# Kernel tuning notes

Hardware: AMD Instinct MI355X
Metric: run time of the kernel (lower is better)

## Reference

```python
import jax, jax.numpy as jnp
import numpy as np


def setup_inputs() -> dict:
    key = jax.random.key(0)
    k_q, k_k, k_v, k_xd, k_yd = jax.random.split(key, 5)
    B, L, H, E, K = 8, 4096, 2048, 512, 64
    return {
        "queries": jax.random.normal(k_q, (B, L, E), dtype=jnp.float32),
        "keys": jax.random.normal(k_k, (B, L, E), dtype=jnp.float32),
        "values": jax.random.normal(k_v, (B, L, E), dtype=jnp.float32),
        "x_date": jax.random.normal(k_xd, (B, L, K), dtype=jnp.float32),
        "y_date": jax.random.normal(k_yd, (B, H, K), dtype=jnp.float32),
    }


def reference(queries, keys, values, x_date, y_date):
    # queries/keys are unused in the original forward's math (only shapes).
    k = x_date.shape[-1]
    scale = 1.0 / float(np.sqrt(k))  # self.scale is None -> 1/sqrt(k)
    # scores: [B, L, H] from date features
    scores = jnp.einsum('blk,bhk->blh', x_date, y_date)
    # softmax over target axis H (dim=-1), numerically stable
    A = jax.nn.softmax(scale * scores, axis=-1)  # [B, L, H]
    # weighted reduction over source axis L -> [B, H, E]
    V = jnp.einsum('ble,blh->bhe', values, A)
    return V
```

## Files before the change

kernel.cpp:

```cpp
#include <hip/hip_runtime.h>
#include <hip/hip_bf16.h>

#define BN 8
#define LN 4096
#define HN 2048
#define EN 512
#define KN 64
#define LT 32

typedef __attribute__((ext_vector_type(8))) short bf16x8;
typedef __attribute__((ext_vector_type(4))) float f32x4;

__device__ __forceinline__ short f2b(float x) {
  union { float f; unsigned u; } v; v.f = x;
  unsigned r = v.u + 0x7fffu + ((v.u >> 16) & 1u);
  return (short)(r >> 16);
}

__device__ __forceinline__ void gload16(const void* g, void* s) {
  __builtin_amdgcn_global_load_lds(
      (const __attribute__((address_space(1))) unsigned int*)(unsigned long long)g,
      (__attribute__((address_space(3))) unsigned int*)(unsigned int)(unsigned long long)s,
      16, 0, 0);
}

__global__ __launch_bounds__(256) void prep_cvt(const float* __restrict__ src,
                                                short* __restrict__ dst, float scale) {
  int i = blockIdx.x * 256 + threadIdx.x;
  f32x4 a = *(const f32x4*)(src + (size_t)i * 8);
  f32x4 b = *(const f32x4*)(src + (size_t)i * 8 + 4);
  bf16x8 r;
  r[0] = f2b(a[0] * scale); r[1] = f2b(a[1] * scale);
  r[2] = f2b(a[2] * scale); r[3] = f2b(a[3] * scale);
  r[4] = f2b(b[0] * scale); r[5] = f2b(b[1] * scale);
  r[6] = f2b(b[2] * scale); r[7] = f2b(b[3] * scale);
  *(bf16x8*)(dst + (size_t)i * 8) = r;
}

__global__ __launch_bounds__(256) void prep_v(const float* __restrict__ vals,
                                              short* __restrict__ valsT) {
  __shared__ short tile[64 * 66];
  const int b = blockIdx.z;
  const int l0 = blockIdx.x * 64, e0 = blockIdx.y * 64;
  const int tid = threadIdx.x;
  {
    int lr = tid >> 2, ec = (tid & 3) * 16;
    const float* src = vals + ((size_t)b * LN + l0 + lr) * EN + e0 + ec;
    short* trow = tile + lr * 66 + ec;
#pragma unroll
    for (int q = 0; q < 4; ++q) {
      f32x4 v = *(const f32x4*)(src + q * 4);
      unsigned u0 = (unsigned)(unsigned short)f2b(v[0]) | ((unsigned)(unsigned short)f2b(v[1]) << 16);
      unsigned u1 = (unsigned)(unsigned short)f2b(v[2]) | ((unsigned)(unsigned short)f2b(v[3]) << 16);
      *(unsigned*)(trow + q * 4) = u0;
      *(unsigned*)(trow + q * 4 + 2) = u1;
    }
  }
  __syncthreads();
  {
    int er = tid >> 2, lc = (tid & 3) * 16;
    union { short s[16]; bf16x8 v[2]; } u;
#pragma unroll
    for (int k2 = 0; k2 < 16; ++k2) u.s[k2] = tile[(lc + k2) * 66 + er];
    short* dst = valsT + ((size_t)b * EN + e0 + er) * LN + l0 + lc;
    *(bf16x8*)dst = u.v[0];
    *(bf16x8*)(dst + 8) = u.v[1];
  }
}

__global__ __launch_bounds__(256) void k_stats2(const short* __restrict__ xb,
                                                const short* __restrict__ yb,
                                                float* __restrict__ ps) {
  const int b = blockIdx.y, hc = blockIdx.z;
  const int tid = threadIdx.x, w = tid >> 6, lane = tid & 63;
  const int row = lane & 15, g = lane >> 4;
  const int lb = blockIdx.x * 128 + w * 32;
  const size_t bL = (size_t)b * LN, bH = (size_t)b * HN;

  bf16x8 xa[2][2];
#pragma unroll
  for (int lt = 0; lt < 2; ++lt) {
    const short* xp = xb + ((bL + lb + lt * 16 + row) << 6) + 8 * g;
    xa[lt][0] = *(const bf16x8*)xp;
    xa[lt][1] = *(const bf16x8*)(xp + 32);
  }
  float s[2][4] = {{0.f, 0.f, 0.f, 0.f}, {0.f, 0.f, 0.f, 0.f}};
  const short* ybase = yb + ((bH + hc * 512 + row) << 6) + 8 * g;
#pragma unroll 2
  for (int it = 0; it < 32; ++it) {
    const short* yp = ybase + ((size_t)it << 10);
    bf16x8 y0 = *(const bf16x8*)yp;
    bf16x8 y1 = *(const bf16x8*)(yp + 32);
#pragma unroll
    for (int lt = 0; lt < 2; ++lt) {
      f32x4 a = {0.f, 0.f, 0.f, 0.f};
      a = __builtin_amdgcn_mfma_f32_16x16x32_bf16(xa[lt][0], y0, a, 0, 0, 0);
      a = __builtin_amdgcn_mfma_f32_16x16x32_bf16(xa[lt][1], y1, a, 0, 0, 0);
#pragma unroll
      for (int r = 0; r < 4; ++r) s[lt][r] += __builtin_amdgcn_exp2f(a[r]);
    }
  }
#pragma unroll
  for (int d = 1; d < 16; d <<= 1)
#pragma unroll
    for (int lt = 0; lt < 2; ++lt)
#pragma unroll
      for (int r = 0; r < 4; ++r) s[lt][r] += __shfl_xor(s[lt][r], d);
  if (row == 0) {
#pragma unroll
    for (int lt = 0; lt < 2; ++lt)
#pragma unroll
      for (int r = 0; r < 4; ++r)
        ps[(size_t)hc * (BN * LN) + bL + lb + lt * 16 + 4 * g + r] = s[lt][r];
  }
}

__global__ void k_comb(const float* __restrict__ ps, float* __restrict__ wv) {
  int idx = blockIdx.x * 256 + threadIdx.x;
  float z = ps[idx] + ps[BN * LN + idx] + ps[2 * BN * LN + idx] + ps[3 * BN * LN + idx];
  wv[idx] = 1.0f / z;
}

__global__ __launch_bounds__(256, 4) void k_main2(
    const short* __restrict__ valsT, const short* __restrict__ xb,
    const short* __restrict__ yb, const float* __restrict__ wv,
    float* __restrict__ out) {
  __shared__ __align__(16) char smem[33024];
  const int tid = threadIdx.x;
  const int lane = tid & 63, w = tid >> 6;
  const int row = lane & 15, g = lane >> 4;

  int flat = blockIdx.x + 32 * blockIdx.y + 128 * blockIdx.z;
  int re = (flat & 7) * 128 + (flat >> 3);
  const int hb = (re & 31) * 64;
  const int eb = ((re >> 5) & 3) * 128;
  const int b = re >> 7;
  const size_t bL = (size_t)b * LN, bH = (size_t)b * HN;

  bf16x8 ya[2][2];
#pragma unroll
  for (int j2 = 0; j2 < 2; ++j2) {
    const short* yp = yb + ((bH + hb + ((w >> 1) * 2 + j2) * 16 + row) << 6) + 8 * g;
    ya[j2][0] = *(const bf16x8*)yp;
    ya[j2][1] = *(const bf16x8*)(yp + 32);
  }

  f32x4 acc[2][4];
#pragma unroll
  for (int at = 0; at < 2; ++at)
#pragma unroll
    for (int n = 0; n < 4; ++n) acc[at][n] = (f32x4){0.f, 0.f, 0.f, 0.f};

  const int wbase = __builtin_amdgcn_readfirstlane(tid & ~63);

  auto stage = [&](int buf, int l0n) {
#pragma unroll
    for (int j = 0; j < 2; ++j) {
      int i = j * 256 + tid;
      int e = i >> 2, sl = (i & 3) ^ ((e >> 1) & 3);
      const short* src = valsT + (((size_t)b * EN + eb + e) << 12) + l0n + 8 * sl;
      gload16(src, smem + buf * 8192 + (j * 256 + wbase) * 16);
    }
    {
      int l = tid >> 3, sl = (tid & 7) ^ (l & 7);
      const short* src = xb + ((bL + l0n + l) << 6) + 8 * sl;
      gload16(src, smem + 16384 + buf * 4096 + wbase * 16);
    }
    if (tid < 8) {
      gload16(wv + bL + l0n + 4 * tid, smem + 32768 + buf * 128);
    }
  };

  stage(0, 0);
  __syncthreads();

  const int t = w & 1, hp = w >> 1;
  int cur = 0;
  for (int it = 0; it < LN / LT; ++it) {
    int l0 = it * LT;
    if (it + 1 < LN / LT) stage(cur ^ 1, l0 + LT);

    short* xT = (short*)(smem + 16384 + cur * 4096);
    char* pT = smem + 24576 + cur * 4096;
    float* sw = (float*)(smem + 32768 + cur * 128);

    int sp0 = g ^ (row & 7);
    const short* xrow = xT + ((t * 16 + row) << 6);
    bf16x8 xa0 = *(const bf16x8*)(xrow + (sp0 << 3));
    bf16x8 xa1 = *(const bf16x8*)(xrow + ((sp0 ^ 4) << 3));
    float swv[4];
#pragma unroll
    for (int r = 0; r < 4; ++r) swv[r] = sw[t * 16 + 4 * g + r];
#pragma unroll
    for (int j2 = 0; j2 < 2; ++j2) {
      f32x4 s4 = {0.f, 0.f, 0.f, 0.f};
      s4 = __builtin_amdgcn_mfma_f32_16x16x32_bf16(xa0, ya[j2][0], s4, 0, 0, 0);
      s4 = __builtin_amdgcn_mfma_f32_16x16x32_bf16(xa1, ya[j2][1], s4, 0, 0, 0);
      int hq = (hp * 2 + j2) * 16 + row;
      unsigned u0 = (unsigned)(unsigned short)f2b(__builtin_amdgcn_exp2f(s4[0]) * swv[0]) |
                    ((unsigned)(unsigned short)f2b(__builtin_amdgcn_exp2f(s4[1]) * swv[1]) << 16);
      unsigned u1 = (unsigned)(unsigned short)f2b(__builtin_amdgcn_exp2f(s4[2]) * swv[2]) |
                    ((unsigned)(unsigned short)f2b(__builtin_amdgcn_exp2f(s4[3]) * swv[3]) << 16);
      int sphy = (2 * t + (g >> 1)) ^ ((hq >> 1) & 3);
      *(unsigned long long*)(pT + hq * 64 + sphy * 16 + (g & 1) * 8) =
          (unsigned long long)u0 | ((unsigned long long)u1 << 32);
    }
    __syncthreads();

    char* vT = smem + cur * 8192;
    bf16x8 pa[2];
#pragma unroll
    for (int at = 0; at < 2; ++at) {
      int hq = (w >> 1) * 32 + at * 16 + row;
      pa[at] = *(const bf16x8*)(pT + hq * 64 + ((g ^ ((hq >> 1) & 3)) << 4));
    }
#pragma unroll
    for (int n = 0; n < 4; ++n) {
      int el = (w & 1) * 64 + n * 16 + row;
      bf16x8 vb = *(const bf16x8*)(vT + el * 64 + ((g ^ ((el >> 1) & 3)) << 4));
#pragma unroll
      for (int at = 0; at < 2; ++at)
        acc[at][n] = __builtin_amdgcn_mfma_f32_16x16x32_bf16(pa[at], vb, acc[at][n], 0, 0, 0);
    }
    __syncthreads();
    cur ^= 1;
  }

#pragma unroll
  for (int at = 0; at < 2; ++at)
#pragma unroll
    for (int n = 0; n < 4; ++n)
#pragma unroll
      for (int r = 0; r < 4; ++r) {
        int h = hb + (w >> 1) * 32 + at * 16 + 4 * g + r;
        int e = eb + (w & 1) * 64 + n * 16 + row;
        out[(bH + h) * (size_t)EN + e] = acc[at][n][r];
      }
}

__device__ __forceinline__ bf16x8 cvt8(const float* __restrict__ p) {
  f32x4 a = *(const f32x4*)(p);
  f32x4 b = *(const f32x4*)(p + 4);
  bf16x8 r;
  r[0] = f2b(a[0]); r[1] = f2b(a[1]); r[2] = f2b(a[2]); r[3] = f2b(a[3]);
  r[4] = f2b(b[0]); r[5] = f2b(b[1]); r[6] = f2b(b[2]); r[7] = f2b(b[3]);
  return r;
}

__global__ __launch_bounds__(256) void k_stats_o(const float* __restrict__ xd,
                                                 const float* __restrict__ yd,
                                                 float* __restrict__ mz) {
  const int b = blockIdx.y;
  const int w = threadIdx.x >> 6;
  const int lane = threadIdx.x & 63;
  const int row = lane & 15, g = lane >> 4;
  const int lb = blockIdx.x * 64 + w * 16;
  const float* xp = xd + ((size_t)b * LN + lb + row) * KN + g * 8;
  bf16x8 a0 = cvt8(xp), a1 = cvt8(xp + 32);
  float m[4], s[4];
#pragma unroll
  for (int r = 0; r < 4; ++r) { m[r] = -1e30f; s[r] = 0.f; }
  const float* ybp = yd + ((size_t)b * HN + row) * KN + g * 8;
  for (int h0 = 0; h0 < HN; h0 += 16) {
    bf16x8 b0 = cvt8(ybp + (size_t)h0 * KN);
    bf16x8 b1 = cvt8(ybp + (size_t)h0 * KN + 32);
    f32x4 acc = {0.f, 0.f, 0.f, 0.f};
    acc = __builtin_amdgcn_mfma_f32_16x16x32_bf16(a0, b0, acc, 0, 0, 0);
    acc = __builtin_amdgcn_mfma_f32_16x16x32_bf16(a1, b1, acc, 0, 0, 0);
#pragma unroll
    for (int r = 0; r < 4; ++r) {
      float v = acc[r] * 0.125f;
      float mn = fmaxf(m[r], v);
      s[r] = s[r] * __expf(m[r] - mn) + __expf(v - mn);
      m[r] = mn;
    }
  }
#pragma unroll
  for (int d = 1; d < 16; d <<= 1) {
#pragma unroll
    for (int r = 0; r < 4; ++r) {
      float mo = __shfl_xor(m[r], d);
      float so = __shfl_xor(s[r], d);
      float mn = fmaxf(m[r], mo);
      s[r] = s[r] * __expf(m[r] - mn) + so * __expf(mo - mn);
      m[r] = mn;
    }
  }
  if (row == 0) {
#pragma unroll
    for (int r = 0; r < 4; ++r) {
      size_t idx = (size_t)b * LN + lb + 4 * g + r;
      mz[idx] = m[r];
      mz[(size_t)BN * LN + idx] = 1.0f / s[r];
    }
  }
}

__global__ __launch_bounds__(512) void k_main_o(const float* __restrict__ vals,
                                                const float* __restrict__ xd,
                                                const float* __restrict__ yd,
                                                const float* __restrict__ mz,
                                                float* __restrict__ out) {
  __shared__ short vT[256][34];
  __shared__ short pT[128][34];
  __shared__ short xT[LT][72];
  __shared__ float smm[LT], smz[LT];
  const int b = blockIdx.z;
  const int hb = blockIdx.x * 128;
  const int eb = blockIdx.y * 256;
  const int tid = threadIdx.x;
  const int w = tid >> 6, lane = tid & 63;
  const int row = lane & 15, g = lane >> 4;
  const float* yp = yd + ((size_t)b * HN + hb + w * 16 + row) * KN + g * 8;
  bf16x8 ya0 = cvt8(yp), ya1 = cvt8(yp + 32);
  f32x4 acc[16];
#pragma unroll
  for (int n = 0; n < 16; ++n) acc[n] = (f32x4){0.f, 0.f, 0.f, 0.f};
  const float* mzb = mz + (size_t)b * LN;
  const float* rzb = mz + (size_t)BN * LN + (size_t)b * LN;
  for (int l0 = 0; l0 < LN; l0 += LT) {
    __syncthreads();
    {
      int xl = tid >> 4, xk = (tid & 15) * 4;
      f32x4 xv = *(const f32x4*)(xd + ((size_t)b * LN + l0 + xl) * KN + xk);
      union { short h[4]; int i[2]; } u;
      u.h[0] = f2b(xv[0]); u.h[1] = f2b(xv[1]); u.h[2] = f2b(xv[2]); u.h[3] = f2b(xv[3]);
      int* dst = (int*)(&xT[xl][xk]);
      dst[0] = u.i[0]; dst[1] = u.i[1];
    }
#pragma unroll
    for (int lp = 0; lp < 4; ++lp) {
      int vl = (tid >> 6) + lp * 8;
      const float* vrow = vals + ((size_t)b * LN + l0 + vl) * EN + eb;
#pragma unroll
      for (int u2 = 0; u2 < 4; ++u2) {
        int e = (tid & 63) + u2 * 64;
        vT[e][vl] = f2b(vrow[e]);
      }
    }
    if (tid < LT) { smm[tid] = mzb[l0 + tid]; smz[tid] = rzb[l0 + tid]; }
    __syncthreads();
#pragma unroll
    for (int t2 = 0; t2 < 2; ++t2) {
      const short* xr = &xT[t2 * 16 + row][0];
      bf16x8 xb0 = *(const bf16x8*)(xr + 8 * g);
      bf16x8 xb1 = *(const bf16x8*)(xr + 32 + 8 * g);
      f32x4 sa = {0.f, 0.f, 0.f, 0.f};
      sa = __builtin_amdgcn_mfma_f32_16x16x32_bf16(ya0, xb0, sa, 0, 0, 0);
      sa = __builtin_amdgcn_mfma_f32_16x16x32_bf16(ya1, xb1, sa, 0, 0, 0);
      int lcol = t2 * 16 + row;
      float mm = smm[lcol], zz = smz[lcol];
#pragma unroll
      for (int r = 0; r < 4; ++r) {
        float p = __expf(sa[r] * 0.125f - mm) * zz;
        pT[w * 16 + 4 * g + r][lcol] = f2b(p);
      }
    }
    __syncthreads();
    bf16x8 pa;
    {
      const int* pi = (const int*)(&pT[w * 16 + row][0] + 8 * g);
      union { int i[4]; bf16x8 f; } u;
      u.i[0] = pi[0]; u.i[1] = pi[1]; u.i[2] = pi[2]; u.i[3] = pi[3];
      pa = u.f;
    }
#pragma unroll
    for (int n = 0; n < 16; ++n) {
      const int* vi = (const int*)(&vT[n * 16 + row][0] + 8 * g);
      union { int i[4]; bf16x8 f; } u;
      u.i[0] = vi[0]; u.i[1] = vi[1]; u.i[2] = vi[2]; u.i[3] = vi[3];
      acc[n] = __builtin_amdgcn_mfma_f32_16x16x32_bf16(pa, u.f, acc[n], 0, 0, 0);
    }
  }
#pragma unroll
  for (int n = 0; n < 16; ++n)
#pragma unroll
    for (int r = 0; r < 4; ++r) {
      int h = hb + w * 16 + 4 * g + r;
      int e = eb + n * 16 + row;
      out[((size_t)b * HN + h) * EN + e] = acc[n][r];
    }
}

extern "C" void kernel_launch(void* const* d_in, const int* in_sizes, int n_in,
                              void* d_out, int out_size, void* d_ws, size_t ws_size,
                              hipStream_t stream) {
  const float* vals = (const float*)d_in[2];
  const float* xd = (const float*)d_in[3];
  const float* yd = (const float*)d_in[4];
  float* out = (float*)d_out;

  if (ws_size >= 40501248ull) {
    char* wsb = (char*)d_ws;
    short* valsT = (short*)wsb;
    short* xbuf  = (short*)(wsb + 33554432);
    short* ybuf  = (short*)(wsb + 37748736);
    float* ps    = (float*)(wsb + 39845888);
    float* wv    = (float*)(wsb + 40370176);

    const float c0 = 0.125f * 1.4426950408889634f;
    prep_cvt<<<dim3(BN * LN * KN / 2048), 256, 0, stream>>>(xd, xbuf, c0);
    prep_cvt<<<dim3(BN * HN * KN / 2048), 256, 0, stream>>>(yd, ybuf, 1.0f);
    prep_v<<<dim3(LN / 64, EN / 64, BN), 256, 0, stream>>>(vals, valsT);
    k_stats2<<<dim3(LN / 128, BN, 4), 256, 0, stream>>>(xbuf, ybuf, ps);
    k_comb<<<dim3(BN * LN / 256), 256, 0, stream>>>(ps, wv);
    k_main2<<<dim3(32, 4, 8), 256, 0, stream>>>(valsT, xbuf, ybuf, wv, out);
  } else {
    float* mz = (float*)d_ws;
    k_stats_o<<<dim3(LN / 64, BN), 256, 0, stream>>>(xd, yd, mz);
    k_main_o<<<dim3(HN / 128, EN / 256, BN), 512, 0, stream>>>(vals, xd, yd, mz, out);
  }
}
```

Baseline: 197.6 us.

## Merge prep kernels and widen main kernel with triple-buffered async pipeline

The x and y bf16 conversions now run as one launch, and the values transpose runs as one launch together with the softmax-denominator stats, so fewer kernels are launched and independent work can run concurrently. The main kernel moves to 512-thread blocks covering 256 E columns, which halves the number of times the score/exp tile is recomputed per H tile. It also switches to a three-stage LDS ring, prefetching two tiles ahead, with explicit vmcnt waits in place of full syncthreads. The cost is higher LDS use per block (about 64KB), which may reduce occupancy, and more fragile hand-written wait counts.

```diff
diff --git a/kernel.cpp b/kernel.cpp
--- a/kernel.cpp
+++ b/kernel.cpp
@@ -7,6 +7,7 @@
 #define EN 512
 #define KN 64
 #define LT 32
+#define NIT 128
 
 typedef __attribute__((ext_vector_type(8))) short bf16x8;
 typedef __attribute__((ext_vector_type(4))) float f32x4;
@@ -15,6 +16,15 @@
   union { float f; unsigned u; } v; v.f = x;
   unsigned r = v.u + 0x7fffu + ((v.u >> 16) & 1u);
   return (short)(r >> 16);
+}
+
+__device__ __forceinline__ bf16x8 cvt8(const float* __restrict__ p) {
+  f32x4 a = *(const f32x4*)(p);
+  f32x4 b = *(const f32x4*)(p + 4);
+  bf16x8 r;
+  r[0] = f2b(a[0]); r[1] = f2b(a[1]); r[2] = f2b(a[2]); r[3] = f2b(a[3]);
+  r[4] = f2b(b[0]); r[5] = f2b(b[1]); r[6] = f2b(b[2]); r[7] = f2b(b[3]);
+  return r;
 }
 
 __device__ __forceinline__ void gload16(const void* g, void* s) {
@@ -24,9 +34,22 @@
       16, 0, 0);
 }
 
-__global__ __launch_bounds__(256) void prep_cvt(const float* __restrict__ src,
-                                                short* __restrict__ dst, float scale) {
-  int i = blockIdx.x * 256 + threadIdx.x;
+__global__ __launch_bounds__(256) void prep_cvt2(const float* __restrict__ xs,
+                                                 short* __restrict__ xo,
+                                                 const float* __restrict__ ys,
+                                                 short* __restrict__ yo) {
+  int bx = blockIdx.x;
+  const float* src;
+  short* dst;
+  float scale;
+  int i;
+  if (bx < 1024) {
+    i = bx * 256 + threadIdx.x;
+    src = xs; dst = xo; scale = 0.125f * 1.4426950408889634f;
+  } else {
+    i = (bx - 1024) * 256 + threadIdx.x;
+    src = ys; dst = yo; scale = 1.0f;
+  }
   f32x4 a = *(const f32x4*)(src + (size_t)i * 8);
   f32x4 b = *(const f32x4*)(src + (size_t)i * 8 + 4);
   bf16x8 r;
@@ -37,81 +60,84 @@
   *(bf16x8*)(dst + (size_t)i * 8) = r;
 }
 
-__global__ __launch_bounds__(256) void prep_v(const float* __restrict__ vals,
-                                              short* __restrict__ valsT) {
+__global__ __launch_bounds__(256) void k_pv_stats(const float* __restrict__ vals,
+                                                  short* __restrict__ valsT,
+                                                  const short* __restrict__ xb,
+                                                  const short* __restrict__ yb,
+                                                  float* __restrict__ ps) {
   __shared__ short tile[64 * 66];
-  const int b = blockIdx.z;
-  const int l0 = blockIdx.x * 64, e0 = blockIdx.y * 64;
+  const int bx = blockIdx.x;
   const int tid = threadIdx.x;
-  {
-    int lr = tid >> 2, ec = (tid & 3) * 16;
-    const float* src = vals + ((size_t)b * LN + l0 + lr) * EN + e0 + ec;
-    short* trow = tile + lr * 66 + ec;
-#pragma unroll
-    for (int q = 0; q < 4; ++q) {
-      f32x4 v = *(const f32x4*)(src + q * 4);
-      unsigned u0 = (unsigned)(unsigned short)f2b(v[0]) | ((unsigned)(unsigned short)f2b(v[1]) << 16);
-      unsigned u1 = (unsigned)(unsigned short)f2b(v[2]) | ((unsigned)(unsigned short)f2b(v[3]) << 16);
-      *(unsigned*)(trow + q * 4) = u0;
-      *(unsigned*)(trow + q * 4 + 2) = u1;
-    }
-  }
-  __syncthreads();
-  {
-    int er = tid >> 2, lc = (tid & 3) * 16;
-    union { short s[16]; bf16x8 v[2]; } u;
-#pragma unroll
-    for (int k2 = 0; k2 < 16; ++k2) u.s[k2] = tile[(lc + k2) * 66 + er];
-    short* dst = valsT + ((size_t)b * EN + e0 + er) * LN + l0 + lc;
-    *(bf16x8*)dst = u.v[0];
-    *(bf16x8*)(dst + 8) = u.v[1];
-  }
-}
-
-__global__ __launch_bounds__(256) void k_stats2(const short* __restrict__ xb,
-                                                const short* __restrict__ yb,
-                                                float* __restrict__ ps) {
-  const int b = blockIdx.y, hc = blockIdx.z;
-  const int tid = threadIdx.x, w = tid >> 6, lane = tid & 63;
-  const int row = lane & 15, g = lane >> 4;
-  const int lb = blockIdx.x * 128 + w * 32;
-  const size_t bL = (size_t)b * LN, bH = (size_t)b * HN;
-
-  bf16x8 xa[2][2];
-#pragma unroll
-  for (int lt = 0; lt < 2; ++lt) {
-    const short* xp = xb + ((bL + lb + lt * 16 + row) << 6) + 8 * g;
-    xa[lt][0] = *(const bf16x8*)xp;
-    xa[lt][1] = *(const bf16x8*)(xp + 32);
-  }
-  float s[2][4] = {{0.f, 0.f, 0.f, 0.f}, {0.f, 0.f, 0.f, 0.f}};
-  const short* ybase = yb + ((bH + hc * 512 + row) << 6) + 8 * g;
+  if (bx < 4096) {
+    const int b = bx >> 9;
+    const int e0 = ((bx >> 6) & 7) * 64;
+    const int l0 = (bx & 63) * 64;
+    {
+      int lr = tid >> 2, ec = (tid & 3) * 16;
+      const float* src = vals + ((size_t)b * LN + l0 + lr) * EN + e0 + ec;
+      short* trow = tile + lr * 66 + ec;
+#pragma unroll
+      for (int q = 0; q < 4; ++q) {
+        f32x4 v = *(const f32x4*)(src + q * 4);
+        unsigned u0 = (unsigned)(unsigned short)f2b(v[0]) | ((unsigned)(unsigned short)f2b(v[1]) << 16);
+        unsigned u1 = (unsigned)(unsigned short)f2b(v[2]) | ((unsigned)(unsigned short)f2b(v[3]) << 16);
+        *(unsigned*)(trow + q * 4) = u0;
+        *(unsigned*)(trow + q * 4 + 2) = u1;
+      }
+    }
+    __syncthreads();
+    {
+      int er = tid >> 2, lc = (tid & 3) * 16;
+      union { short s[16]; bf16x8 v[2]; } u;
+#pragma unroll
+      for (int k2 = 0; k2 < 16; ++k2) u.s[k2] = tile[(lc + k2) * 66 + er];
+      short* dst = valsT + ((size_t)b * EN + e0 + er) * LN + l0 + lc;
+      *(bf16x8*)dst = u.v[0];
+      *(bf16x8*)(dst + 8) = u.v[1];
+    }
+  } else {
+    const int idx = bx - 4096;
+    const int b = (idx >> 5) & 7, hc = idx >> 8;
+    const int w = tid >> 6, lane = tid & 63;
+    const int row = lane & 15, g = lane >> 4;
+    const int lb = (idx & 31) * 128 + w * 32;
+    const size_t bL = (size_t)b * LN, bH = (size_t)b * HN;
+    bf16x8 xa[2][2];
+#pragma unroll
+    for (int lt = 0; lt < 2; ++lt) {
+      const short* xp = xb + ((bL + lb + lt * 16 + row) << 6) + 8 * g;
+      xa[lt][0] = *(const bf16x8*)xp;
+      xa[lt][1] = *(const bf16x8*)(xp + 32);
+    }
+    float s[2][4] = {{0.f, 0.f, 0.f, 0.f}, {0.f, 0.f, 0.f, 0.f}};
+    const short* ybase = yb + ((bH + hc * 512 + row) << 6) + 8 * g;
 #pragma unroll 2
-  for (int it = 0; it < 32; ++it) {
-    const short* yp = ybase + ((size_t)it << 10);
-    bf16x8 y0 = *(const bf16x8*)yp;
-    bf16x8 y1 = *(const bf16x8*)(yp + 32);
-#pragma unroll
-    for (int lt = 0; lt < 2; ++lt) {
-      f32x4 a = {0.f, 0.f, 0.f, 0.f};
-      a = __builtin_amdgcn_mfma_f32_16x16x32_bf16(xa[lt][0], y0, a, 0, 0, 0);
-      a = __builtin_amdgcn_mfma_f32_16x16x32_bf16(xa[lt][1], y1, a, 0, 0, 0);
-#pragma unroll
-      for (int r = 0; r < 4; ++r) s[lt][r] += __builtin_amdgcn_exp2f(a[r]);
-    }
-  }
-#pragma unroll
-  for (int d = 1; d < 16; d <<= 1)
-#pragma unroll
-    for (int lt = 0; lt < 2; ++lt)
-#pragma unroll
-      for (int r = 0; r < 4; ++r) s[lt][r] += __shfl_xor(s[lt][r], d);
-  if (row == 0) {
-#pragma unroll
-    for (int lt = 0; lt < 2; ++lt)
-#pragma unroll
-      for (int r = 0; r < 4; ++r)
-        ps[(size_t)hc * (BN * LN) + bL + lb + lt * 16 + 4 * g + r] = s[lt][r];
+    for (int it = 0; it < 32; ++it) {
+      const short* yp = ybase + ((size_t)it << 10);
+      bf16x8 y0 = *(const bf16x8*)yp;
+      bf16x8 y1 = *(const bf16x8*)(yp + 32);
+#pragma unroll
+      for (int lt = 0; lt < 2; ++lt) {
+        f32x4 a = {0.f, 0.f, 0.f, 0.f};
+        a = __builtin_amdgcn_mfma_f32_16x16x32_bf16(xa[lt][0], y0, a, 0, 0, 0);
+        a = __builtin_amdgcn_mfma_f32_16x16x32_bf16(xa[lt][1], y1, a, 0, 0, 0);
+#pragma unroll
+        for (int r = 0; r < 4; ++r) s[lt][r] += __builtin_amdgcn_exp2f(a[r]);
+      }
+    }
+#pragma unroll
+    for (int d = 1; d < 16; d <<= 1)
+#pragma unroll
+      for (int lt = 0; lt < 2; ++lt)
+#pragma unroll
+        for (int r = 0; r < 4; ++r) s[lt][r] += __shfl_xor(s[lt][r], d);
+    if (row == 0) {
+#pragma unroll
+      for (int lt = 0; lt < 2; ++lt)
+#pragma unroll
+        for (int r = 0; r < 4; ++r)
+          ps[(size_t)hc * (BN * LN) + bL + lb + lt * 16 + 4 * g + r] = s[lt][r];
+    }
   }
 }
 
@@ -121,28 +147,71 @@
   wv[idx] = 1.0f / z;
 }
 
-__global__ __launch_bounds__(256, 4) void k_main2(
+__global__ __launch_bounds__(512, 4) void k_main3(
     const short* __restrict__ valsT, const short* __restrict__ xb,
     const short* __restrict__ yb, const float* __restrict__ wv,
     float* __restrict__ out) {
-  __shared__ __align__(16) char smem[33024];
+  __shared__ __align__(16) char smem[65920];
   const int tid = threadIdx.x;
-  const int lane = tid & 63, w = tid >> 6;
+  const int w = tid >> 6, lane = tid & 63;
   const int row = lane & 15, g = lane >> 4;
 
-  int flat = blockIdx.x + 32 * blockIdx.y + 128 * blockIdx.z;
-  int re = (flat & 7) * 128 + (flat >> 3);
-  const int hb = (re & 31) * 64;
-  const int eb = ((re >> 5) & 3) * 128;
-  const int b = re >> 7;
+  const int f = blockIdx.x;
+  const int b = f & 7;
+  const int rest = f >> 3;
+  const int hb = (rest & 31) * 64;
+  const int eb = (rest >> 5) * 256;
   const size_t bL = (size_t)b * LN, bH = (size_t)b * HN;
 
-  bf16x8 ya[2][2];
-#pragma unroll
-  for (int j2 = 0; j2 < 2; ++j2) {
-    const short* yp = yb + ((bH + hb + ((w >> 1) * 2 + j2) * 16 + row) << 6) + 8 * g;
-    ya[j2][0] = *(const bf16x8*)yp;
-    ya[j2][1] = *(const bf16x8*)(yp + 32);
+  const int wbase = __builtin_amdgcn_readfirstlane(tid & ~63);
+
+  const short* vsrc[2];
+#pragma unroll
+  for (int j = 0; j < 2; ++j) {
+    int i = j * 512 + tid;
+    int e = i >> 2, sl = (i & 3) ^ ((e >> 1) & 3);
+    vsrc[j] = valsT + (((size_t)b * EN + eb + e) << 12) + 8 * sl;
+  }
+  const short* xsrc;
+  {
+    int p = w * 32 + (lane & 31);
+    int l = p >> 3, sl = (p & 7) ^ (l & 7);
+    xsrc = xb + ((bL + l) << 6) + 8 * sl;
+  }
+  const float* ssrc = wv + bL + 4 * tid;
+
+  auto stage = [&](int buf, int tl) {
+    int loff = tl * 32;
+#pragma unroll
+    for (int j = 0; j < 2; ++j)
+      gload16(vsrc[j] + loff, smem + buf * 16384 + (j * 8192 + wbase * 16));
+    if (lane < 32)
+      gload16(xsrc + loff * 64, smem + 49152 + buf * 4096 + wbase * 8);
+    if (tid < 8)
+      gload16(ssrc + loff, smem + 65536 + buf * 128);
+  };
+
+  const int ht = w >> 1, lt = w & 1;
+  bf16x8 ya0, ya1;
+  {
+    const short* yp = yb + ((bH + hb + ht * 16 + row) << 6) + 8 * g;
+    ya0 = *(const bf16x8*)yp;
+    ya1 = *(const bf16x8*)(yp + 32);
+  }
+  const int sp0 = g ^ (row & 7);
+  const int xoffA = ((lt * 16 + row) << 7) + (sp0 << 4);
+  const int xoffB = ((lt * 16 + row) << 7) + ((sp0 ^ 4) << 4);
+  const int swoff = (lt * 16 + 4 * g) * 4;
+  const int hq1 = ht * 16 + row;
+  const int poff_w = hq1 * 64 + (((2 * lt + (g >> 1)) ^ ((hq1 >> 1) & 3)) << 4) + (g & 1) * 8;
+  const int hq2a = (w >> 2) * 32 + row, hq2b = hq2a + 16;
+  const int paoffA = hq2a * 64 + ((g ^ ((hq2a >> 1) & 3)) << 4);
+  const int paoffB = hq2b * 64 + ((g ^ ((hq2b >> 1) & 3)) << 4);
+  int vboff[4];
+#pragma unroll
+  for (int n = 0; n < 4; ++n) {
+    int el = (w & 3) * 64 + n * 16 + row;
+    vboff[n] = el * 64 + ((g ^ ((el >> 1) & 3)) << 4);
   }
 
   f32x4 acc[2][4];
@@ -151,79 +220,55 @@
 #pragma unroll
     for (int n = 0; n < 4; ++n) acc[at][n] = (f32x4){0.f, 0.f, 0.f, 0.f};
 
-  const int wbase = __builtin_amdgcn_readfirstlane(tid & ~63);
-
-  auto stage = [&](int buf, int l0n) {
-#pragma unroll
-    for (int j = 0; j < 2; ++j) {
-      int i = j * 256 + tid;
-      int e = i >> 2, sl = (i & 3) ^ ((e >> 1) & 3);
-      const short* src = valsT + (((size_t)b * EN + eb + e) << 12) + l0n + 8 * sl;
-      gload16(src, smem + buf * 8192 + (j * 256 + wbase) * 16);
-    }
-    {
-      int l = tid >> 3, sl = (tid & 7) ^ (l & 7);
-      const short* src = xb + ((bL + l0n + l) << 6) + 8 * sl;
-      gload16(src, smem + 16384 + buf * 4096 + wbase * 16);
-    }
-    if (tid < 8) {
-      gload16(wv + bL + l0n + 4 * tid, smem + 32768 + buf * 128);
-    }
-  };
-
   stage(0, 0);
-  __syncthreads();
-
-  const int t = w & 1, hp = w >> 1;
-  int cur = 0;
-  for (int it = 0; it < LN / LT; ++it) {
-    int l0 = it * LT;
-    if (it + 1 < LN / LT) stage(cur ^ 1, l0 + LT);
-
-    short* xT = (short*)(smem + 16384 + cur * 4096);
-    char* pT = smem + 24576 + cur * 4096;
-    float* sw = (float*)(smem + 32768 + cur * 128);
-
-    int sp0 = g ^ (row & 7);
-    const short* xrow = xT + ((t * 16 + row) << 6);
-    bf16x8 xa0 = *(const bf16x8*)(xrow + (sp0 << 3));
-    bf16x8 xa1 = *(const bf16x8*)(xrow + ((sp0 ^ 4) << 3));
-    float swv[4];
-#pragma unroll
-    for (int r = 0; r < 4; ++r) swv[r] = sw[t * 16 + 4 * g + r];
-#pragma unroll
-    for (int j2 = 0; j2 < 2; ++j2) {
+  stage(1, 1);
+  asm volatile("s_waitcnt vmcnt(3)" ::: "memory");
+  __builtin_amdgcn_s_barrier();
+  asm volatile("" ::: "memory");
+
+  int rb = 0, sb = 2;
+  for (int it = 0; it < NIT; ++it) {
+    if (it + 2 < NIT) stage(sb, it + 2);
+
+    {
+      const char* xbuf = smem + 49152 + rb * 4096;
+      bf16x8 xa0 = *(const bf16x8*)(xbuf + xoffA);
+      bf16x8 xa1 = *(const bf16x8*)(xbuf + xoffB);
+      f32x4 sws = *(const f32x4*)(smem + 65536 + rb * 128 + swoff);
       f32x4 s4 = {0.f, 0.f, 0.f, 0.f};
-      s4 = __builtin_amdgcn_mfma_f32_16x16x32_bf16(xa0, ya[j2][0], s4, 0, 0, 0);
-      s4 = __builtin_amdgcn_mfma_f32_16x16x32_bf16(xa1, ya[j2][1], s4, 0, 0, 0);
-      int hq = (hp * 2 + j2) * 16 + row;
-      unsigned u0 = (unsigned)(unsigned short)f2b(__builtin_amdgcn_exp2f(s4[0]) * swv[0]) |
-                    ((unsigned)(unsigned short)f2b(__builtin_amdgcn_exp2f(s4[1]) * swv[1]) << 16);
-      unsigned u1 = (unsigned)(unsigned short)f2b(__builtin_amdgcn_exp2f(s4[2]) * swv[2]) |
-                    ((unsigned)(unsigned short)f2b(__builtin_amdgcn_exp2f(s4[3]) * swv[3]) << 16);
-      int sphy = (2 * t + (g >> 1)) ^ ((hq >> 1) & 3);
-      *(unsigned long long*)(pT + hq * 64 + sphy * 16 + (g & 1) * 8) =
+      s4 = __builtin_amdgcn_mfma_f32_16x16x32_bf16(xa0, ya0, s4, 0, 0, 0);
+      s4 = __builtin_amdgcn_mfma_f32_16x16x32_bf16(xa1, ya1, s4, 0, 0, 0);
+      unsigned u0 = (unsigned)(unsigned short)f2b(__builtin_amdgcn_exp2f(s4[0]) * sws[0]) |
+                    ((unsigned)(unsigned short)f2b(__builtin_amdgcn_exp2f(s4[1]) * sws[1]) << 16);
+      unsigned u1 = (unsigned)(unsigned short)f2b(__builtin_amdgcn_exp2f(s4[2]) * sws[2]) |
+                    ((unsigned)(unsigned short)f2b(__builtin_amdgcn_exp2f(s4[3]) * sws[3]) << 16);
+      *(unsigned long long*)(smem + 61440 + poff_w) =
           (unsigned long long)u0 | ((unsigned long long)u1 << 32);
     }
-    __syncthreads();
-
-    char* vT = smem + cur * 8192;
-    bf16x8 pa[2];
-#pragma unroll
-    for (int at = 0; at < 2; ++at) {
-      int hq = (w >> 1) * 32 + at * 16 + row;
-      pa[at] = *(const bf16x8*)(pT + hq * 64 + ((g ^ ((hq >> 1) & 3)) << 4));
-    }
-#pragma unroll
-    for (int n = 0; n < 4; ++n) {
-      int el = (w & 1) * 64 + n * 16 + row;
-      bf16x8 vb = *(const bf16x8*)(vT + el * 64 + ((g ^ ((el >> 1) & 3)) << 4));
-#pragma unroll
-      for (int at = 0; at < 2; ++at)
-        acc[at][n] = __builtin_amdgcn_mfma_f32_16x16x32_bf16(pa[at], vb, acc[at][n], 0, 0, 0);
-    }
-    __syncthreads();
-    cur ^= 1;
+    asm volatile("s_waitcnt lgkmcnt(0)" ::: "memory");
+    __builtin_amdgcn_s_barrier();
+    asm volatile("" ::: "memory");
+
+    {
+      const char* vbuf = smem + rb * 16384;
+      bf16x8 pa0 = *(const bf16x8*)(smem + 61440 + paoffA);
+      bf16x8 pa1 = *(const bf16x8*)(smem + 61440 + paoffB);
+#pragma unroll
+      for (int n = 0; n < 4; ++n) {
+        bf16x8 vb = *(const bf16x8*)(vbuf + vboff[n]);
+        acc[0][n] = __builtin_amdgcn_mfma_f32_16x16x32_bf16(pa0, vb, acc[0][n], 0, 0, 0);
+        acc[1][n] = __builtin_amdgcn_mfma_f32_16x16x32_bf16(pa1, vb, acc[1][n], 0, 0, 0);
+      }
+    }
+    if (it < NIT - 2)
+      asm volatile("s_waitcnt vmcnt(3) lgkmcnt(0)" ::: "memory");
+    else
+      asm volatile("s_waitcnt vmcnt(0) lgkmcnt(0)" ::: "memory");
+    __builtin_amdgcn_s_barrier();
+    asm volatile("" ::: "memory");
+
+    rb = rb == 2 ? 0 : rb + 1;
+    sb = sb == 2 ? 0 : sb + 1;
   }
 
 #pragma unroll
@@ -232,19 +277,10 @@
     for (int n = 0; n < 4; ++n)
 #pragma unroll
       for (int r = 0; r < 4; ++r) {
-        int h = hb + (w >> 1) * 32 + at * 16 + 4 * g + r;
-        int e = eb + (w & 1) * 64 + n * 16 + row;
+        int h = hb + (w >> 2) * 32 + at * 16 + 4 * g + r;
+        int e = eb + (w & 3) * 64 + n * 16 + row;
         out[(bH + h) * (size_t)EN + e] = acc[at][n][r];
       }
-}
-
-__device__ __forceinline__ bf16x8 cvt8(const float* __restrict__ p) {
-  f32x4 a = *(const f32x4*)(p);
-  f32x4 b = *(const f32x4*)(p + 4);
-  bf16x8 r;
-  r[0] = f2b(a[0]); r[1] = f2b(a[1]); r[2] = f2b(a[2]); r[3] = f2b(a[3]);
-  r[4] = f2b(b[0]); r[5] = f2b(b[1]); r[6] = f2b(b[2]); r[7] = f2b(b[3]);
-  return r;
 }
 
 __global__ __launch_bounds__(256) void k_stats_o(const float* __restrict__ xd,
@@ -398,13 +434,10 @@
     float* ps    = (float*)(wsb + 39845888);
     float* wv    = (float*)(wsb + 40370176);
 
-    const float c0 = 0.125f * 1.4426950408889634f;
-    prep_cvt<<<dim3(BN * LN * KN / 2048), 256, 0, stream>>>(xd, xbuf, c0);
-    prep_cvt<<<dim3(BN * HN * KN / 2048), 256, 0, stream>>>(yd, ybuf, 1.0f);
-    prep_v<<<dim3(LN / 64, EN / 64, BN), 256, 0, stream>>>(vals, valsT);
-    k_stats2<<<dim3(LN / 128, BN, 4), 256, 0, stream>>>(xbuf, ybuf, ps);
+    prep_cvt2<<<dim3(1536), 256, 0, stream>>>(xd, xbuf, yd, ybuf);
+    k_pv_stats<<<dim3(5120), 256, 0, stream>>>(vals, valsT, xbuf, ybuf, ps);
     k_comb<<<dim3(BN * LN / 256), 256, 0, stream>>>(ps, wv);
-    k_main2<<<dim3(32, 4, 8), 256, 0, stream>>>(valsT, xbuf, ybuf, wv, out);
+    k_main3<<<dim3(512), 512, 0, stream>>>(valsT, xbuf, ybuf, wv, out);
   } else {
     float* mz = (float*)d_ws;
     k_stats_o<<<dim3(LN / 64, BN), 256, 0, stream>>>(xd, yd, mz);
```

Result: faster. 182.2 us (-7.8%).
